# Kernel tuning notes

Hardware: AMD Instinct MI355X
Metric: run time of the kernel (lower is better)

Reference implementation:

```python
import jax, jax.numpy as jnp
import numpy as np

L, T, F, DIM = 16, 16384, 2, 3
N_MIN, N_MAX = 16.0, 512.0
N_PTS = 262144
# torch code builds np.int32 primes [1, 2654435761, 805459861]; 2654435761 wraps to -1640531535.
# Since T is a power of two, int32 wraparound multiply/xor followed by nonnegative mod T gives
# bit-identical indices to the int64 torch computation.
PIS = jnp.array([1, -1640531535, 805459861], dtype=jnp.int32)
# corner ordering from get_indices: corner k = a*4+b*2+c with a->dim0, b->dim1, c->dim2
OFFS = jnp.array([[(k >> 2) & 1, (k >> 1) & 1, k & 1] for k in range(8)], dtype=jnp.float32)  # (8,3)


def setup_inputs() -> dict:
    key = jax.random.key(0)
    k1, k2 = jax.random.split(key)
    x = jax.random.uniform(k1, (N_PTS, DIM), dtype=jnp.float32)
    # nn.init.uniform_(weight, a=-1e-4, b=1e-4) for each of L tables of shape (T, F)
    embeddings = jax.random.uniform(k2, (L, T, F), minval=-1e-4, maxval=1e-4, dtype=jnp.float32)
    return {"x": x, "embeddings": embeddings}


def reference(x, embeddings):
    # per-level growth factor b = exp((log Nmax - log Nmin)/L); N_l = Nmin * b**l
    b = jnp.exp((jnp.log(N_MAX) - jnp.log(N_MIN)) / L)
    N_l = N_MIN * b ** jnp.arange(L, dtype=jnp.float32)                      # (L,)
    un_x = x[None, :, :] * N_l[:, None, None]                                # (L,N,3)  (mu=0, sigma=1)
    lo = jnp.floor(un_x)
    hi = jnp.ceil(un_x)
    d = hi - lo                                                              # (L,N,3)
    nz = d != 0
    diff = jnp.where(nz, (un_x - lo) / jnp.where(nz, d, 1.0), 0.0)           # (L,N,3)

    mask = OFFS.astype(bool)[None, None]                                     # (1,1,8,3)
    corners = jnp.where(mask, hi[:, :, None, :], lo[:, :, None, :])          # (L,N,8,3)
    ci = corners.astype(jnp.int32)
    prod = ci * PIS                                                          # (L,N,8,3) wrapping int32 mul
    idx = jnp.mod(prod[..., 0] ^ prod[..., 1] ^ prod[..., 2], T)             # (L,N,8)

    # per-level table gather: (L,T,F)[ (L,N,8) ] -> (L,N,8,F)
    feats = jax.vmap(lambda emb, i: emb[i])(embeddings, idx)

    # trilinear weights: prod over dims of (diff if corner bit else 1-diff)
    w = jnp.prod(jnp.where(mask, diff[:, :, None, :], 1.0 - diff[:, :, None, :]), axis=-1)  # (L,N,8)
    c = jnp.einsum('lnc,lncf->lnf', w, feats)                                # (L,N,F)
    return jnp.transpose(c, (1, 0, 2)).reshape(x.shape[0], L * F)            # (N, L*F)
```

## Files before the change

### kernel.cpp

```cpp
#include <hip/hip_runtime.h>
#include <stdint.h>

constexpr int L_LEVELS = 16;
constexpr int T_SIZE   = 16384;
constexpr int N_PTS    = 262144;

typedef _Float16 h2 __attribute__((ext_vector_type(2)));
typedef _Float16 h4 __attribute__((ext_vector_type(4)));
typedef _Float16 h8 __attribute__((ext_vector_type(8)));

constexpr uint32_t P1_4 = 2654435761u * 4u;
constexpr uint32_t P2_4 = 805459861u * 4u;
constexpr uint32_t M4   = (T_SIZE - 1) * 4u;

__device__ __forceinline__ h2 lerp2(h2 a, h2 b, h2 t) {
    return a + t * (b - a);
}

__global__ __launch_bounds__(256) void cvt_tables(
    const float* __restrict__ emb, h2* __restrict__ tbl)
{
    const int i = blockIdx.x * 256 + threadIdx.x;
    const float4* __restrict__ s = reinterpret_cast<const float4*>(emb);
    float4 a = s[2 * i];
    float4 b = s[2 * i + 1];
    h8 w = { (_Float16)a.x, (_Float16)a.y, (_Float16)a.z, (_Float16)a.w,
             (_Float16)b.x, (_Float16)b.y, (_Float16)b.z, (_Float16)b.w };
    reinterpret_cast<h8*>(tbl)[i] = w;
}

__global__ __launch_bounds__(1024, 4) void hash_encode_fused(
    const float* __restrict__ x,
    const h2*    __restrict__ tbl,
    float4*      __restrict__ out)
{
    __shared__ union {
        h2 tab[2][T_SIZE];
        h2 tr[1024][20];
    } sm;

    const int t = threadIdx.x;
    const int n = blockIdx.x * 1024 + t;

    const int rot = (blockIdx.x << 4) & 4095;

    const float x0 = x[3 * n + 0];
    const float x1 = x[3 * n + 1];
    const float x2 = x[3 * n + 2];

    {
        const h8* __restrict__ s = reinterpret_cast<const h8*>(tbl);
        h8* __restrict__ d = reinterpret_cast<h8*>(sm.tab[0]);
#pragma unroll
        for (int r = 0; r < 4; ++r) {
            const int j = (r * 1024 + t + rot) & 4095;
            d[j] = s[j];
        }
    }
    __syncthreads();

    union { h2 r[L_LEVELS]; h8 q[4]; } res;

#pragma unroll
    for (int l = 0; l < L_LEVELS; ++l) {
        h8 stg0, stg1, stg2, stg3;
        int j0 = 0, j1 = 0, j2 = 0, j3 = 0;
        if (l < L_LEVELS - 1) {
            const h8* __restrict__ s =
                reinterpret_cast<const h8*>(tbl + (size_t)(l + 1) * T_SIZE);
            j0 = (0 * 1024 + t + rot) & 4095;
            j1 = (1 * 1024 + t + rot) & 4095;
            j2 = (2 * 1024 + t + rot) & 4095;
            j3 = (3 * 1024 + t + rot) & 4095;
            stg0 = s[j0];
            stg1 = s[j1];
            stg2 = s[j2];
            stg3 = s[j3];
        }

        const float Nl = 16.0f * exp2f((float)l * 0.3125f);
        const char* __restrict__ tb =
            reinterpret_cast<const char*>(sm.tab[l & 1]);

        const float u0 = x0 * Nl, u1 = x1 * Nl, u2 = x2 * Nl;
        const float fl0 = floorf(u0), fl1 = floorf(u1), fl2 = floorf(u2);
        const float df0 = u0 - fl0, df1 = u1 - fl1, df2 = u2 - fl2;

        const uint32_t q0 = ((uint32_t)(int32_t)fl0) << 2;
        const uint32_t q1 = ((uint32_t)(int32_t)fl1) * P1_4;
        const uint32_t q2 = ((uint32_t)(int32_t)fl2) * P2_4;
        const uint32_t d0 = (q0 ^ (q0 + 4u))   & M4;
        const uint32_t d1 = (q1 ^ (q1 + P1_4)) & M4;
        const uint32_t d2 = (q2 ^ (q2 + P2_4)) & M4;

        uint32_t off = (q0 ^ q1 ^ q2) & M4;

        constexpr int gray[8] = {0, 1, 3, 2, 6, 7, 5, 4};
        h2 f[8];
#pragma unroll
        for (int j = 0; j < 8; ++j) {
            f[gray[j]] = *reinterpret_cast<const h2*>(tb + off);
            if (j < 7) {
                const int tog = gray[j] ^ gray[j + 1];
                off ^= (tog == 4) ? d0 : (tog == 2) ? d1 : d2;
            }
        }

        const _Float16 h0 = (_Float16)df0, h1 = (_Float16)df1, hv2 = (_Float16)df2;
        const h2 t0 = {h0, h0}, t1 = {h1, h1}, t2 = {hv2, hv2};
        h2 e0 = lerp2(f[0], f[1], t2);
        h2 e1 = lerp2(f[2], f[3], t2);
        h2 e2 = lerp2(f[4], f[5], t2);
        h2 e3 = lerp2(f[6], f[7], t2);
        h2 g0 = lerp2(e0, e1, t1);
        h2 g1 = lerp2(e2, e3, t1);
        res.r[l] = lerp2(g0, g1, t0);

        if (l < L_LEVELS - 1) {
            h8* __restrict__ d = reinterpret_cast<h8*>(sm.tab[(l + 1) & 1]);
            d[j0] = stg0;
            d[j1] = stg1;
            d[j2] = stg2;
            d[j3] = stg3;
            __syncthreads();
        }
    }

    __syncthreads();
#pragma unroll
    for (int g = 0; g < 4; ++g)
        *reinterpret_cast<h8*>(&sm.tr[t][4 * g]) = res.q[g];
    __syncthreads();

    float4* __restrict__ o = out + (size_t)blockIdx.x * 8192;
#pragma unroll
    for (int i = 0; i < 8; ++i) {
        const int p  = i * 128 + (t >> 3);
        const int l0 = 2 * (t & 7);
        h4 v = *reinterpret_cast<const h4*>(&sm.tr[p][l0]);
        o[i * 1024 + t] = make_float4((float)v.x, (float)v.y,
                                      (float)v.z, (float)v.w);
    }
}

__global__ __launch_bounds__(512, 4) void hash_encode_lds_direct(
    const float* __restrict__ x,
    const float* __restrict__ emb,
    float2* __restrict__ dst)
{
    __shared__ h2 tab[T_SIZE];

    const int l     = blockIdx.x & (L_LEVELS - 1);
    const int chunk = blockIdx.x >> 4;
    const int t     = threadIdx.x;
    const int n0    = chunk * 4096 + t * 8;

    {
        const float4* __restrict__ src =
            reinterpret_cast<const float4*>(emb + (size_t)l * T_SIZE * 2);
        h8* __restrict__ d8 = reinterpret_cast<h8*>(tab);
#pragma unroll
        for (int it = 0; it < 8; ++it) {
            const int i = it * 512 + t;
            float4 a = src[2 * i];
            float4 b = src[2 * i + 1];
            h8 w = { (_Float16)a.x, (_Float16)a.y, (_Float16)a.z, (_Float16)a.w,
                     (_Float16)b.x, (_Float16)b.y, (_Float16)b.z, (_Float16)b.w };
            d8[i] = w;
        }
    }

    union { float4 q[6]; float f[24]; } xs;
    {
        const float4* __restrict__ xv =
            reinterpret_cast<const float4*>(x + (size_t)n0 * 3);
#pragma unroll
        for (int i = 0; i < 6; ++i) xs.q[i] = xv[i];
    }

    __syncthreads();

    const float Nl = 16.0f * exp2f((float)l * 0.3125f);
    const char* __restrict__ tb = reinterpret_cast<const char*>(tab);

#pragma unroll
    for (int p = 0; p < 8; ++p) {
        const float u0 = xs.f[3 * p + 0] * Nl;
        const float u1 = xs.f[3 * p + 1] * Nl;
        const float u2 = xs.f[3 * p + 2] * Nl;

        const float fl0 = floorf(u0), fl1 = floorf(u1), fl2 = floorf(u2);
        const float df0 = u0 - fl0, df1 = u1 - fl1, df2 = u2 - fl2;

        const uint32_t q0 = ((uint32_t)(int32_t)fl0) << 2;
        const uint32_t q1 = ((uint32_t)(int32_t)fl1) * P1_4;
        const uint32_t q2 = ((uint32_t)(int32_t)fl2) * P2_4;
        const uint32_t d0 = (q0 ^ (q0 + 4u))   & M4;
        const uint32_t d1 = (q1 ^ (q1 + P1_4)) & M4;
        const uint32_t d2 = (q2 ^ (q2 + P2_4)) & M4;

        uint32_t off = (q0 ^ q1 ^ q2) & M4;

        constexpr int gray[8] = {0, 1, 3, 2, 6, 7, 5, 4};
        h2 f[8];
#pragma unroll
        for (int j = 0; j < 8; ++j) {
            f[gray[j]] = *reinterpret_cast<const h2*>(tb + off);
            if (j < 7) {
                const int tog = gray[j] ^ gray[j + 1];
                off ^= (tog == 4) ? d0 : (tog == 2) ? d1 : d2;
            }
        }

        const _Float16 h0 = (_Float16)df0, h1 = (_Float16)df1, hv2 = (_Float16)df2;
        const h2 t0 = {h0, h0}, t1 = {h1, h1}, t2 = {hv2, hv2};
        h2 e0 = lerp2(f[0], f[1], t2);
        h2 e1 = lerp2(f[2], f[3], t2);
        h2 e2 = lerp2(f[4], f[5], t2);
        h2 e3 = lerp2(f[6], f[7], t2);
        h2 g0 = lerp2(e0, e1, t1);
        h2 g1 = lerp2(e2, e3, t1);
        h2 r  = lerp2(g0, g1, t0);
        dst[(size_t)(n0 + p) * L_LEVELS + l] =
            make_float2((float)r.x, (float)r.y);
    }
}

extern "C" void kernel_launch(void* const* d_in, const int* in_sizes, int n_in,
                              void* d_out, int out_size, void* d_ws, size_t ws_size,
                              hipStream_t stream) {
    const float* x   = (const float*)d_in[0];
    const float* emb = (const float*)d_in[1];

    const size_t tbl_bytes = (size_t)L_LEVELS * T_SIZE * sizeof(h2);

    if (ws_size >= tbl_bytes) {
        cvt_tables<<<256, 256, 0, stream>>>(emb, (h2*)d_ws);
        hash_encode_fused<<<256, 1024, 0, stream>>>(x, (const h2*)d_ws,
                                                    (float4*)d_out);
    } else {
        hash_encode_lds_direct<<<1024, 512, 0, stream>>>(x, emb,
                                                         (float2*)d_out);
    }
}
```

Before: 94.36 us.

## Split hash encoding into level-group blocks plus a separate transpose kernel

Replaces the single fused kernel, where each block walks all 16 levels, with a kernel whose blocks each handle 4 levels for 4096 points. It writes fp16 per-level results to a workspace buffer, and a second kernel transposes them and expands them to fp32 output. This spreads the sequential per-level table staging over more independent blocks, each doing 8 points per thread. The cost is an extra launch and an intermediate round trip through global memory of 16 MB. The fallback path now fuses table conversion into the fused kernel in place of the old direct kernel.

```diff
diff --git a/kernel.cpp b/kernel.cpp
--- a/kernel.cpp
+++ b/kernel.cpp
@@ -16,6 +16,7 @@
 __device__ __forceinline__ h2 lerp2(h2 a, h2 b, h2 t) {
     return a + t * (b - a);
 }
+
 
 __global__ __launch_bounds__(256) void cvt_tables(
     const float* __restrict__ emb, h2* __restrict__ tbl)
@@ -29,9 +30,142 @@
     reinterpret_cast<h8*>(tbl)[i] = w;
 }
 
+__global__ __launch_bounds__(512, 2) void hash_encode_groups(
+    const float* __restrict__ x,
+    const h2*    __restrict__ tbl,
+    h2*          __restrict__ res)
+{
+    __shared__ h2 tab[2][T_SIZE];
+
+    const int t     = threadIdx.x;
+    const int chunk = blockIdx.x & 63;
+    const int L0    = (blockIdx.x >> 6) * 4;
+    const int n0    = chunk * 4096 + t * 8;
+
+    {
+        const h8* __restrict__ s =
+            reinterpret_cast<const h8*>(tbl + (size_t)L0 * T_SIZE);
+        h8* __restrict__ d = reinterpret_cast<h8*>(tab[0]);
+#pragma unroll
+        for (int r = 0; r < 8; ++r) {
+            const int j = r * 512 + t;
+            d[j] = s[j];
+        }
+    }
+
+    union { float4 q[6]; float f[24]; } xs;
+    {
+        const float4* __restrict__ xv =
+            reinterpret_cast<const float4*>(x + (size_t)n0 * 3);
+#pragma unroll
+        for (int i = 0; i < 6; ++i) xs.q[i] = xv[i];
+    }
+    __syncthreads();
+
+#pragma unroll
+    for (int l = 0; l < 4; ++l) {
+        h8 stg[8];
+        if (l < 3) {
+            const h8* __restrict__ s = reinterpret_cast<const h8*>(
+                tbl + (size_t)(L0 + l + 1) * T_SIZE);
+#pragma unroll
+            for (int r = 0; r < 8; ++r) stg[r] = s[r * 512 + t];
+        }
+
+        const float Nl = 16.0f * exp2f((float)(L0 + l) * 0.3125f);
+        const char* __restrict__ tb =
+            reinterpret_cast<const char*>(tab[l & 1]);
+
+        union { h2 r[8]; float4 q[2]; } out8;
+
+#pragma unroll
+        for (int p = 0; p < 8; ++p) {
+            const float u0 = xs.f[3 * p + 0] * Nl;
+            const float u1 = xs.f[3 * p + 1] * Nl;
+            const float u2 = xs.f[3 * p + 2] * Nl;
+
+            const float fl0 = floorf(u0), fl1 = floorf(u1), fl2 = floorf(u2);
+            const float df0 = u0 - fl0, df1 = u1 - fl1, df2 = u2 - fl2;
+
+            const uint32_t q0 = ((uint32_t)(int32_t)fl0) << 2;
+            const uint32_t q1 = ((uint32_t)(int32_t)fl1) * P1_4;
+            const uint32_t q2 = ((uint32_t)(int32_t)fl2) * P2_4;
+            const uint32_t d0 = (q0 ^ (q0 + 4u))   & M4;
+            const uint32_t d1 = (q1 ^ (q1 + P1_4)) & M4;
+            const uint32_t d2 = (q2 ^ (q2 + P2_4)) & M4;
+
+            uint32_t off = (q0 ^ q1 ^ q2) & M4;
+
+            constexpr int gray[8] = {0, 1, 3, 2, 6, 7, 5, 4};
+            h2 f[8];
+#pragma unroll
+            for (int j = 0; j < 8; ++j) {
+                f[gray[j]] = *reinterpret_cast<const h2*>(tb + off);
+                if (j < 7) {
+                    const int tog = gray[j] ^ gray[j + 1];
+                    off ^= (tog == 4) ? d0 : (tog == 2) ? d1 : d2;
+                }
+            }
+
+            const _Float16 h0 = (_Float16)df0, h1 = (_Float16)df1,
+                           hv2 = (_Float16)df2;
+            const h2 t0 = {h0, h0}, t1 = {h1, h1}, t2 = {hv2, hv2};
+            h2 e0 = lerp2(f[0], f[1], t2);
+            h2 e1 = lerp2(f[2], f[3], t2);
+            h2 e2 = lerp2(f[4], f[5], t2);
+            h2 e3 = lerp2(f[6], f[7], t2);
+            h2 g0 = lerp2(e0, e1, t1);
+            h2 g1 = lerp2(e2, e3, t1);
+            out8.r[p] = lerp2(g0, g1, t0);
+        }
+
+        {
+            float4* __restrict__ o4 = reinterpret_cast<float4*>(
+                res + (size_t)(L0 + l) * N_PTS + n0);
+            o4[0] = out8.q[0];
+            o4[1] = out8.q[1];
+        }
+
+        if (l < 3) {
+            h8* __restrict__ d = reinterpret_cast<h8*>(tab[(l + 1) & 1]);
+#pragma unroll
+            for (int r = 0; r < 8; ++r) d[r * 512 + t] = stg[r];
+            __syncthreads();
+        }
+    }
+}
+
+__global__ __launch_bounds__(256) void transpose_expand(
+    const h2* __restrict__ res,
+    float4*   __restrict__ out)
+{
+    __shared__ h2 tile[L_LEVELS][514];
+    const int t    = threadIdx.x;
+    const int base = blockIdx.x * 512;
+
+#pragma unroll
+    for (int l = 0; l < L_LEVELS; ++l) {
+        h4 v = reinterpret_cast<const h4*>(res + (size_t)l * N_PTS + base)[t];
+        *reinterpret_cast<h4*>(&tile[l][2 * t]) = v;
+    }
+    __syncthreads();
+
+    float4* __restrict__ o = out + (size_t)base * 8;
+#pragma unroll
+    for (int i = 0; i < L_LEVELS; ++i) {
+        const int f    = i * 256 + t;
+        const int p    = f >> 3;
+        const int part = f & 7;
+        h2 a = tile[2 * part][p];
+        h2 b = tile[2 * part + 1][p];
+        o[f] = make_float4((float)a.x, (float)a.y,
+                           (float)b.x, (float)b.y);
+    }
+}
+
 __global__ __launch_bounds__(1024, 4) void hash_encode_fused(
     const float* __restrict__ x,
-    const h2*    __restrict__ tbl,
+    const float* __restrict__ emb,
     float4*      __restrict__ out)
 {
     __shared__ union {
@@ -41,7 +175,6 @@
 
     const int t = threadIdx.x;
     const int n = blockIdx.x * 1024 + t;
-
     const int rot = (blockIdx.x << 4) & 4095;
 
     const float x0 = x[3 * n + 0];
@@ -49,33 +182,37 @@
     const float x2 = x[3 * n + 2];
 
     {
-        const h8* __restrict__ s = reinterpret_cast<const h8*>(tbl);
+        const float4* __restrict__ s = reinterpret_cast<const float4*>(emb);
         h8* __restrict__ d = reinterpret_cast<h8*>(sm.tab[0]);
 #pragma unroll
         for (int r = 0; r < 4; ++r) {
             const int j = (r * 1024 + t + rot) & 4095;
-            d[j] = s[j];
-        }
-    }
-    __syncthreads();
-
-    union { h2 r[L_LEVELS]; h8 q[4]; } res;
+            float4 a = s[2 * j];
+            float4 b = s[2 * j + 1];
+            h8 w = { (_Float16)a.x, (_Float16)a.y, (_Float16)a.z, (_Float16)a.w,
+                     (_Float16)b.x, (_Float16)b.y, (_Float16)b.z, (_Float16)b.w };
+            d[j] = w;
+        }
+    }
+    __syncthreads();
+
+    union { h2 r[L_LEVELS]; h8 q[4]; } resu;
 
 #pragma unroll
     for (int l = 0; l < L_LEVELS; ++l) {
-        h8 stg0, stg1, stg2, stg3;
+        float4 sa0, sb0, sa1, sb1, sa2, sb2, sa3, sb3;
         int j0 = 0, j1 = 0, j2 = 0, j3 = 0;
         if (l < L_LEVELS - 1) {
-            const h8* __restrict__ s =
-                reinterpret_cast<const h8*>(tbl + (size_t)(l + 1) * T_SIZE);
+            const float4* __restrict__ s = reinterpret_cast<const float4*>(
+                emb + (size_t)(l + 1) * T_SIZE * 2);
             j0 = (0 * 1024 + t + rot) & 4095;
             j1 = (1 * 1024 + t + rot) & 4095;
             j2 = (2 * 1024 + t + rot) & 4095;
             j3 = (3 * 1024 + t + rot) & 4095;
-            stg0 = s[j0];
-            stg1 = s[j1];
-            stg2 = s[j2];
-            stg3 = s[j3];
+            sa0 = s[2 * j0]; sb0 = s[2 * j0 + 1];
+            sa1 = s[2 * j1]; sb1 = s[2 * j1 + 1];
+            sa2 = s[2 * j2]; sb2 = s[2 * j2 + 1];
+            sa3 = s[2 * j3]; sb3 = s[2 * j3 + 1];
         }
 
         const float Nl = 16.0f * exp2f((float)l * 0.3125f);
@@ -114,14 +251,22 @@
         h2 e3 = lerp2(f[6], f[7], t2);
         h2 g0 = lerp2(e0, e1, t1);
         h2 g1 = lerp2(e2, e3, t1);
-        res.r[l] = lerp2(g0, g1, t0);
+        resu.r[l] = lerp2(g0, g1, t0);
 
         if (l < L_LEVELS - 1) {
             h8* __restrict__ d = reinterpret_cast<h8*>(sm.tab[(l + 1) & 1]);
-            d[j0] = stg0;
-            d[j1] = stg1;
-            d[j2] = stg2;
-            d[j3] = stg3;
+            h8 w0 = { (_Float16)sa0.x, (_Float16)sa0.y, (_Float16)sa0.z, (_Float16)sa0.w,
+                      (_Float16)sb0.x, (_Float16)sb0.y, (_Float16)sb0.z, (_Float16)sb0.w };
+            h8 w1 = { (_Float16)sa1.x, (_Float16)sa1.y, (_Float16)sa1.z, (_Float16)sa1.w,
+                      (_Float16)sb1.x, (_Float16)sb1.y, (_Float16)sb1.z, (_Float16)sb1.w };
+            h8 w2 = { (_Float16)sa2.x, (_Float16)sa2.y, (_Float16)sa2.z, (_Float16)sa2.w,
+                      (_Float16)sb2.x, (_Float16)sb2.y, (_Float16)sb2.z, (_Float16)sb2.w };
+            h8 w3 = { (_Float16)sa3.x, (_Float16)sa3.y, (_Float16)sa3.z, (_Float16)sa3.w,
+                      (_Float16)sb3.x, (_Float16)sb3.y, (_Float16)sb3.z, (_Float16)sb3.w };
+            d[j0] = w0;
+            d[j1] = w1;
+            d[j2] = w2;
+            d[j3] = w3;
             __syncthreads();
         }
     }
@@ -129,7 +274,7 @@
     __syncthreads();
 #pragma unroll
     for (int g = 0; g < 4; ++g)
-        *reinterpret_cast<h8*>(&sm.tr[t][4 * g]) = res.q[g];
+        *reinterpret_cast<h8*>(&sm.tr[t][4 * g]) = resu.q[g];
     __syncthreads();
 
     float4* __restrict__ o = out + (size_t)blockIdx.x * 8192;
@@ -143,103 +288,22 @@
     }
 }
 
-__global__ __launch_bounds__(512, 4) void hash_encode_lds_direct(
-    const float* __restrict__ x,
-    const float* __restrict__ emb,
-    float2* __restrict__ dst)
-{
-    __shared__ h2 tab[T_SIZE];
-
-    const int l     = blockIdx.x & (L_LEVELS - 1);
-    const int chunk = blockIdx.x >> 4;
-    const int t     = threadIdx.x;
-    const int n0    = chunk * 4096 + t * 8;
-
-    {
-        const float4* __restrict__ src =
-            reinterpret_cast<const float4*>(emb + (size_t)l * T_SIZE * 2);
-        h8* __restrict__ d8 = reinterpret_cast<h8*>(tab);
-#pragma unroll
-        for (int it = 0; it < 8; ++it) {
-            const int i = it * 512 + t;
-            float4 a = src[2 * i];
-            float4 b = src[2 * i + 1];
-            h8 w = { (_Float16)a.x, (_Float16)a.y, (_Float16)a.z, (_Float16)a.w,
-                     (_Float16)b.x, (_Float16)b.y, (_Float16)b.z, (_Float16)b.w };
-            d8[i] = w;
-        }
-    }
-
-    union { float4 q[6]; float f[24]; } xs;
-    {
-        const float4* __restrict__ xv =
-            reinterpret_cast<const float4*>(x + (size_t)n0 * 3);
-#pragma unroll
-        for (int i = 0; i < 6; ++i) xs.q[i] = xv[i];
-    }
-
-    __syncthreads();
-
-    const float Nl = 16.0f * exp2f((float)l * 0.3125f);
-    const char* __restrict__ tb = reinterpret_cast<const char*>(tab);
-
-#pragma unroll
-    for (int p = 0; p < 8; ++p) {
-        const float u0 = xs.f[3 * p + 0] * Nl;
-        const float u1 = xs.f[3 * p + 1] * Nl;
-        const float u2 = xs.f[3 * p + 2] * Nl;
-
-        const float fl0 = floorf(u0), fl1 = floorf(u1), fl2 = floorf(u2);
-        const float df0 = u0 - fl0, df1 = u1 - fl1, df2 = u2 - fl2;
-
-        const uint32_t q0 = ((uint32_t)(int32_t)fl0) << 2;
-        const uint32_t q1 = ((uint32_t)(int32_t)fl1) * P1_4;
-        const uint32_t q2 = ((uint32_t)(int32_t)fl2) * P2_4;
-        const uint32_t d0 = (q0 ^ (q0 + 4u))   & M4;
-        const uint32_t d1 = (q1 ^ (q1 + P1_4)) & M4;
-        const uint32_t d2 = (q2 ^ (q2 + P2_4)) & M4;
-
-        uint32_t off = (q0 ^ q1 ^ q2) & M4;
-
-        constexpr int gray[8] = {0, 1, 3, 2, 6, 7, 5, 4};
-        h2 f[8];
-#pragma unroll
-        for (int j = 0; j < 8; ++j) {
-            f[gray[j]] = *reinterpret_cast<const h2*>(tb + off);
-            if (j < 7) {
-                const int tog = gray[j] ^ gray[j + 1];
-                off ^= (tog == 4) ? d0 : (tog == 2) ? d1 : d2;
-            }
-        }
-
-        const _Float16 h0 = (_Float16)df0, h1 = (_Float16)df1, hv2 = (_Float16)df2;
-        const h2 t0 = {h0, h0}, t1 = {h1, h1}, t2 = {hv2, hv2};
-        h2 e0 = lerp2(f[0], f[1], t2);
-        h2 e1 = lerp2(f[2], f[3], t2);
-        h2 e2 = lerp2(f[4], f[5], t2);
-        h2 e3 = lerp2(f[6], f[7], t2);
-        h2 g0 = lerp2(e0, e1, t1);
-        h2 g1 = lerp2(e2, e3, t1);
-        h2 r  = lerp2(g0, g1, t0);
-        dst[(size_t)(n0 + p) * L_LEVELS + l] =
-            make_float2((float)r.x, (float)r.y);
-    }
-}
-
 extern "C" void kernel_launch(void* const* d_in, const int* in_sizes, int n_in,
                               void* d_out, int out_size, void* d_ws, size_t ws_size,
                               hipStream_t stream) {
     const float* x   = (const float*)d_in[0];
     const float* emb = (const float*)d_in[1];
 
-    const size_t tbl_bytes = (size_t)L_LEVELS * T_SIZE * sizeof(h2);
-
-    if (ws_size >= tbl_bytes) {
-        cvt_tables<<<256, 256, 0, stream>>>(emb, (h2*)d_ws);
-        hash_encode_fused<<<256, 1024, 0, stream>>>(x, (const h2*)d_ws,
-                                                    (float4*)d_out);
+    const size_t RES_OFF = (size_t)2 << 20;
+    const size_t need    = RES_OFF + (size_t)L_LEVELS * N_PTS * sizeof(h2);
+
+    if (ws_size >= need) {
+        h2* tbl = (h2*)d_ws;
+        h2* res = (h2*)((char*)d_ws + RES_OFF);
+        cvt_tables<<<256, 256, 0, stream>>>(emb, tbl);
+        hash_encode_groups<<<256, 512, 0, stream>>>(x, tbl, res);
+        transpose_expand<<<512, 256, 0, stream>>>(res, (float4*)d_out);
     } else {
-        hash_encode_lds_direct<<<1024, 512, 0, stream>>>(x, emb,
-                                                         (float2*)d_out);
-    }
-}
+        hash_encode_fused<<<256, 1024, 0, stream>>>(x, emb, (float4*)d_out);
+    }
+}
```

Measured after the change: 89.69 us. -5.0%, faster.
